# Optimization experiments

Hardware: AMD Instinct MI355X
Metric: run time of the kernel (lower is better)

Reference implementation:

```python
import jax, jax.numpy as jnp
import numpy as np

NU = 50000   # num user nodes
NI = 50000   # num item nodes
E = 1600000  # edges per relation
DIN = 256    # in_features
H = 8        # n_heads
F = 64       # out_features per head (hidden = H*F = 512)
NEG_SLOPE = 0.2


def setup_inputs() -> dict:
    key = jax.random.key(0)
    ks = jax.random.split(key, 14)
    wscale = 0.05
    return {
        "x_user": jax.random.normal(ks[0], (NU, DIN), jnp.float32),
        "x_item": jax.random.normal(ks[1], (NI, DIN), jnp.float32),
        "Wv": jax.random.normal(ks[2], (3, DIN, H * F), jnp.float32) * wscale,
        "bv": jax.random.normal(ks[3], (3, H * F), jnp.float32) * wscale,
        "Wq": jax.random.normal(ks[4], (3, H * F, H), jnp.float32) * wscale,
        "bq": jax.random.normal(ks[5], (3, H), jnp.float32) * wscale,
        "Wk": jax.random.normal(ks[6], (3, H * F, H), jnp.float32) * wscale,
        "bk": jax.random.normal(ks[7], (3, H), jnp.float32) * wscale,
        "src1": jax.random.randint(ks[8], (E,), 0, NU, jnp.int32),   # user -> item
        "dst1": jax.random.randint(ks[9], (E,), 0, NI, jnp.int32),
        "src2": jax.random.randint(ks[10], (E,), 0, NI, jnp.int32),  # item -> user
        "dst2": jax.random.randint(ks[11], (E,), 0, NU, jnp.int32),
        "src3": jax.random.randint(ks[12], (E,), 0, NU, jnp.int32),  # user -> user
        "dst3": jax.random.randint(ks[13], (E,), 0, NU, jnp.int32),
    }


def _gat_relation(x_src, x_dst, Wv, bv, Wq, bq, Wk, bk, src, dst, n_dst):
    # linear_v on src and dst node features: [N, H*F]
    h_src = x_src @ Wv + bv
    h_dst = x_dst @ Wv + bv
    q = h_dst @ Wq + bq  # [Nd, H] per-head query logit
    k = h_src @ Wk + bk  # [Ns, H] per-head key logit
    # fused_gsddmm: gather to edges, leaky_relu, segment softmax over dst
    e = jax.nn.leaky_relu(q[dst] + k[src], NEG_SLOPE)  # [E, H]
    m = jax.ops.segment_max(e, dst, num_segments=n_dst)  # [Nd, H]
    m = jnp.where(jnp.isfinite(m), m, jnp.zeros_like(m))
    ex = jnp.exp(e - m[dst])
    denom = jax.ops.segment_sum(ex, dst, num_segments=n_dst)  # [Nd, H]
    attn = ex / jnp.maximum(denom[dst], 1e-9)  # [E, H]
    # gspmm: attention-weighted scatter-sum of src features into dst
    hs = h_src.reshape(-1, H, F)  # [Ns, H, F]
    agg = jax.ops.segment_sum(attn[:, :, None] * hs[src], dst, num_segments=n_dst)  # [Nd, H, F]
    return agg.mean(axis=1)  # torch.mean(h, dim=1) -> [Nd, F]


def reference(x_user, x_item, Wv, bv, Wq, bq, Wk, bk, src1, dst1, src2, dst2, src3, dst3):
    # relation 0: user -> item
    out_item = _gat_relation(x_user, x_item, Wv[0], bv[0], Wq[0], bq[0], Wk[0], bk[0], src1, dst1, NI)
    # relations 1 (item -> user) and 2 (user -> user) both target user: mean over relations
    r1 = _gat_relation(x_item, x_user, Wv[1], bv[1], Wq[1], bq[1], Wk[1], bk[1], src2, dst2, NU)
    r2 = _gat_relation(x_user, x_user, Wv[2], bv[2], Wq[2], bq[2], Wk[2], bk[2], src3, dst3, NU)
    out_user = (r1 + r2) / 2.0
    return out_user, out_item
```

## Files before the change

### kernel.cpp

```cpp
#include <hip/hip_runtime.h>

typedef unsigned short u16;
typedef __attribute__((ext_vector_type(4))) float f32x4;
typedef __attribute__((ext_vector_type(8))) short s16x8;

#define NND 50000
#define EDG 1600000
#define NBK 391
#define TOTB (3 * NBK)
#define TS 4096
#define CAPB 5120

__device__ __forceinline__ u16 f2b(float f) {
  union { float f; unsigned u; } c; c.f = f;
  unsigned r = c.u + 0x7fff + ((c.u >> 16) & 1);
  return (u16)(r >> 16);
}

__device__ __forceinline__ void accum8(float* num, uint4 u, float4 w0, float4 w1) {
  num[0] += w0.x * __int_as_float((int)(u.x << 16));
  num[1] += w0.y * __int_as_float((int)(u.x & 0xFFFF0000u));
  num[2] += w0.z * __int_as_float((int)(u.y << 16));
  num[3] += w0.w * __int_as_float((int)(u.y & 0xFFFF0000u));
  num[4] += w1.x * __int_as_float((int)(u.z << 16));
  num[5] += w1.y * __int_as_float((int)(u.z & 0xFFFF0000u));
  num[6] += w1.z * __int_as_float((int)(u.w << 16));
  num[7] += w1.w * __int_as_float((int)(u.w & 0xFFFF0000u));
}

__global__ void k_prepw(const float* __restrict__ Wv, u16* __restrict__ Wt,
                        float* __restrict__ Wvt, int* __restrict__ bcur) {
  int tid = blockIdx.x * 256 + threadIdx.x;
  if (tid < 3 * 512 * 256) {
    int r = tid / (512 * 256); int rem = tid - r * 512 * 256;
    int n = rem >> 8; int kk = rem & 255;
    float v = Wv[((size_t)r * 256 + kk) * 512 + n];
    Wt[tid] = f2b(v);
    Wvt[tid] = v;
  }
  if (tid < TOTB) bcur[tid] = tid * CAPB;
}

__global__ void __launch_bounds__(256) k_fusew2(
    const float* __restrict__ Wvt, const float* __restrict__ bv,
    const float* __restrict__ Wq, const float* __restrict__ bq,
    const float* __restrict__ Wk, const float* __restrict__ bk,
    float* __restrict__ FW, float* __restrict__ FB) {
  __shared__ float red[256];
  int r = blockIdx.x >> 4, o = blockIdx.x & 15;
  int t = threadIdx.x;
  const float* wvt = Wvt + (size_t)r * 512 * 256;
  const float* wqk = (o < 8) ? (Wq + (size_t)r * 512 * 8 + o) : (Wk + (size_t)r * 512 * 8 + (o - 8));
  float acc = 0.f;
#pragma unroll 8
  for (int j = 0; j < 512; j++) acc += wvt[(size_t)j * 256 + t] * wqk[j * 8];
  FW[((size_t)r * 16 + o) * 256 + t] = acc;
  float pb = 0.f;
  for (int j = t; j < 512; j += 256) pb += bv[r * 512 + j] * wqk[j * 8];
  red[t] = pb;
  __syncthreads();
  for (int off = 128; off > 0; off >>= 1) {
    if (t < off) red[t] += red[t + off];
    __syncthreads();
  }
  if (t == 0) {
    float b = (o < 8) ? bq[r * 8 + o] : bk[r * 8 + (o - 8)];
    FB[r * 16 + o] = red[0] + b;
  }
}

__global__ void __launch_bounds__(256) kb_scatter(
    const int* __restrict__ s1, const int* __restrict__ d1,
    const int* __restrict__ s2, const int* __restrict__ d2,
    const int* __restrict__ s3, const int* __restrict__ d3,
    int* __restrict__ BCUR, unsigned* __restrict__ pairs) {
  __shared__ int h[NBK];
  __shared__ int bbase[NBK];
  int tid = threadIdx.x;
  int r = blockIdx.y;
  const int* dp = (r == 0) ? d1 : (r == 1) ? d2 : d3;
  const int* sp = (r == 0) ? s1 : (r == 1) ? s2 : s3;
  int e0 = blockIdx.x * TS;
  int n = EDG - e0; if (n > TS) n = TS;
  for (int b = tid; b < NBK; b += 256) h[b] = 0;
  __syncthreads();
  int eb[16]; unsigned ev[16];
#pragma unroll
  for (int k = 0; k < 16; k++) {
    int i = k * 256 + tid;
    if (i < n) {
      int d = dp[e0 + i], ss = sp[e0 + i];
      eb[k] = d >> 7;
      ev[k] = ((unsigned)(d & 127) << 16) | (unsigned)ss;
      atomicAdd(&h[eb[k]], 1);
    } else eb[k] = -1;
  }
  __syncthreads();
  for (int b = tid; b < NBK; b += 256) {
    int c = h[b];
    bbase[b] = c ? atomicAdd(&BCUR[r * NBK + b], c) : 0;
  }
  __syncthreads();
  for (int b = tid; b < NBK; b += 256) h[b] = 0;
  __syncthreads();
#pragma unroll
  for (int k = 0; k < 16; k++) {
    if (eb[k] >= 0) {
      int off = atomicAdd(&h[eb[k]], 1);
      int pos = bbase[eb[k]] + off;
      int limit = (r * NBK + eb[k] + 1) * CAPB;
      if (pos < limit) pairs[pos] = ev[k];
    }
  }
}

__global__ void __launch_bounds__(256) kb_build(
    const unsigned* __restrict__ pairs, const int* __restrict__ BCUR,
    int* __restrict__ rp, int* __restrict__ dgarr, u16* __restrict__ csrc) {
  __shared__ int cntl[128];
  __shared__ int sc[128];
  __shared__ int curl[128];
  int t = threadIdx.x;
  int r = blockIdx.y, bx = blockIdx.x;
  int bin = r * NBK + bx;
  int base = bin * CAPB;
  int cnt = BCUR[bin] - base; if (cnt > CAPB) cnt = CAPB;
  int node0 = bx << 7;
  int nloc = NND - node0; if (nloc > 128) nloc = 128;
  if (t < 128) cntl[t] = 0;
  __syncthreads();
  for (int i = t; i < cnt; i += 256)
    atomicAdd(&cntl[pairs[base + i] >> 16], 1);
  __syncthreads();
  if (t < 128) sc[t] = cntl[t];
  __syncthreads();
  for (int off = 1; off < 128; off <<= 1) {
    int v = 0;
    if (t < 128) { v = sc[t]; if (t >= off) v += sc[t - off]; }
    __syncthreads();
    if (t < 128) sc[t] = v;
    __syncthreads();
  }
  if (t < 128) {
    int excl = sc[t] - cntl[t];
    if (t < nloc) { rp[r * NND + node0 + t] = base + excl; dgarr[r * NND + node0 + t] = cntl[t]; }
    curl[t] = base + excl;
  }
  __syncthreads();
  for (int i = t; i < cnt; i += 256) {
    unsigned v = pairs[base + i];
    int p = atomicAdd(&curl[v >> 16], 1);
    csrc[p] = (u16)(v & 0xFFFFu);
  }
}

__global__ void __launch_bounds__(256) k_gemm(const float* __restrict__ A, const u16* __restrict__ Bt,
                                              const float* __restrict__ bias, u16* __restrict__ C, int M) {
  __shared__ u16 sA[128 * 72];
  __shared__ u16 sB[128 * 72];
  int tid = threadIdx.x;
  int lane = tid & 63, wid = tid >> 6;
  int wm = wid >> 1, wn = wid & 1;
  int l15 = lane & 15, l4 = lane >> 4;
  int m0 = blockIdx.x * 128, n0 = blockIdx.y * 128;
  f32x4 acc[4][4] = {};
  for (int ko = 0; ko < 256; ko += 64) {
#pragma unroll
    for (int p = 0; p < 4; p++) {
      int idx = p * 256 + tid;
      int row = idx >> 3, seg = idx & 7;
      int gm = m0 + row; if (gm >= M) gm = M - 1;
      float4 a0 = *(const float4*)(A + (size_t)gm * 256 + ko + seg * 8);
      float4 a1 = *(const float4*)(A + (size_t)gm * 256 + ko + seg * 8 + 4);
      s16x8 av;
      av[0] = (short)f2b(a0.x); av[1] = (short)f2b(a0.y);
      av[2] = (short)f2b(a0.z); av[3] = (short)f2b(a0.w);
      av[4] = (short)f2b(a1.x); av[5] = (short)f2b(a1.y);
      av[6] = (short)f2b(a1.z); av[7] = (short)f2b(a1.w);
      *(s16x8*)&sA[row * 72 + seg * 8] = av;
      *(s16x8*)&sB[row * 72 + seg * 8] = *(const s16x8*)(Bt + (n0 + row) * 256 + ko + seg * 8);
    }
    __syncthreads();
#pragma unroll
    for (int kk = 0; kk < 2; kk++) {
      s16x8 af[4], bf[4];
#pragma unroll
      for (int i = 0; i < 4; i++) af[i] = *(const s16x8*)&sA[(wm * 64 + i * 16 + l15) * 72 + kk * 32 + l4 * 8];
#pragma unroll
      for (int j = 0; j < 4; j++) bf[j] = *(const s16x8*)&sB[(wn * 64 + j * 16 + l15) * 72 + kk * 32 + l4 * 8];
#pragma unroll
      for (int i = 0; i < 4; i++)
#pragma unroll
        for (int j = 0; j < 4; j++)
          acc[i][j] = __builtin_amdgcn_mfma_f32_16x16x32_bf16(af[i], bf[j], acc[i][j], 0, 0, 0);
    }
    __syncthreads();
  }
#pragma unroll
  for (int j = 0; j < 4; j++) {
    int n = n0 + wn * 64 + j * 16 + l15;
    float bb = bias[n];
    int tpos = ((n & 63) << 3) + (n >> 6);
#pragma unroll
    for (int i = 0; i < 4; i++) {
      int mb = m0 + wm * 64 + i * 16 + l4 * 4;
#pragma unroll
      for (int r = 0; r < 4; r++) {
        int m = mb + r;
        if (m < M) C[(size_t)m * 512 + tpos] = f2b(acc[i][j][r] + bb);
      }
    }
  }
}

__global__ void __launch_bounds__(256) k_qk(
    const float* __restrict__ xu, const float* __restrict__ xi,
    const float* __restrict__ FW, const float* __restrict__ FB,
    float* __restrict__ K0, float* __restrict__ Q1, float* __restrict__ Q2,
    float* __restrict__ K2, float* __restrict__ Q0, float* __restrict__ K1) {
  int lane = threadIdx.x & 63, wid = threadIdx.x >> 6;
  if (blockIdx.x < 1024) {
    int stride = 1024 * 4;
    for (int row = blockIdx.x * 4 + wid; row < NND; row += stride) {
      float4 xv = *(const float4*)(xu + (size_t)row * 256 + lane * 4);
      {
        float p[16];
#pragma unroll
        for (int c = 0; c < 16; c++) {
          const float4 wv = *(const float4*)(FW + (size_t)(8 + c) * 256 + lane * 4);
          p[c] = xv.x * wv.x + xv.y * wv.y + xv.z * wv.z + xv.w * wv.w;
        }
#pragma unroll
        for (int off = 1; off < 64; off <<= 1)
#pragma unroll
          for (int c = 0; c < 16; c++) p[c] += __shfl_xor(p[c], off, 64);
        if (lane == 0) {
#pragma unroll
          for (int c = 0; c < 8; c++) K0[row * 8 + c] = p[c] + FB[8 + c];
#pragma unroll
          for (int c = 0; c < 8; c++) Q1[row * 8 + c] = p[8 + c] + FB[16 + c];
        }
      }
      {
        float p[16];
#pragma unroll
        for (int c = 0; c < 16; c++) {
          const float4 wv = *(const float4*)(FW + (size_t)(32 + c) * 256 + lane * 4);
          p[c] = xv.x * wv.x + xv.y * wv.y + xv.z * wv.z + xv.w * wv.w;
        }
#pragma unroll
        for (int off = 1; off < 64; off <<= 1)
#pragma unroll
          for (int c = 0; c < 16; c++) p[c] += __shfl_xor(p[c], off, 64);
        if (lane == 0) {
#pragma unroll
          for (int c = 0; c < 8; c++) Q2[row * 8 + c] = p[c] + FB[32 + c];
#pragma unroll
          for (int c = 0; c < 8; c++) K2[row * 8 + c] = p[8 + c] + FB[40 + c];
        }
      }
    }
  } else {
    int b = blockIdx.x - 1024;
    int stride = 512 * 4;
    for (int row = b * 4 + wid; row < NND; row += stride) {
      float4 xv = *(const float4*)(xi + (size_t)row * 256 + lane * 4);
      float p[16];
#pragma unroll
      for (int c = 0; c < 16; c++) {
        const float4 wv = *(const float4*)(FW + (size_t)((c < 8) ? c : (16 + c)) * 256 + lane * 4);
        p[c] = xv.x * wv.x + xv.y * wv.y + xv.z * wv.z + xv.w * wv.w;
      }
#pragma unroll
      for (int off = 1; off < 64; off <<= 1)
#pragma unroll
        for (int c = 0; c < 16; c++) p[c] += __shfl_xor(p[c], off, 64);
      if (lane == 0) {
#pragma unroll
        for (int c = 0; c < 8; c++) Q0[row * 8 + c] = p[c] + FB[c];
#pragma unroll
        for (int c = 0; c < 8; c++) K1[row * 8 + c] = p[8 + c] + FB[24 + c];
      }
    }
  }
}

__global__ void __launch_bounds__(256) k_edge(
    const int* __restrict__ rp, const int* __restrict__ dg, const u16* __restrict__ csrc,
    const float* __restrict__ q, const float* __restrict__ k,
    const u16* __restrict__ hs, float* __restrict__ out,
    float scale, int accum) {
  __shared__ float exw[4][64 * 8];
  __shared__ int sarr[4][64];
  __shared__ float sd[4][8];
  __shared__ float sacc[4][64];
  int lane = threadIdx.x & 63, w = threadIdx.x >> 6;
  int dst = blockIdx.x * 2 + (w >> 1);
  int half = w & 1;
  int beg = rp[dst];
  int deg = dg[dst];
  int hlen = (deg + 1) >> 1;
  int s0 = half ? hlen : 0;
  int s1 = half ? deg : hlen;
  float qv[8];
  {
    float4 q0 = *(const float4*)(q + dst * 8);
    float4 q1 = *(const float4*)(q + dst * 8 + 4);
    qv[0] = q0.x; qv[1] = q0.y; qv[2] = q0.z; qv[3] = q0.w;
    qv[4] = q1.x; qv[5] = q1.y; qv[6] = q1.z; qv[7] = q1.w;
  }
  float num[8] = {0, 0, 0, 0, 0, 0, 0, 0};
  float dsum[8] = {0, 0, 0, 0, 0, 0, 0, 0};
  for (int base = s0; base < s1; base += 64) {
    int i = base + lane;
    int nn = min(64, s1 - base);
    if (i < s1) {
      int s = (int)csrc[beg + i];
      sarr[w][lane] = s;
      float4 k0 = *(const float4*)(k + s * 8);
      float4 k1 = *(const float4*)(k + s * 8 + 4);
      float kv[8] = {k0.x, k0.y, k0.z, k0.w, k1.x, k1.y, k1.z, k1.w};
#pragma unroll
      for (int h = 0; h < 8; h++) {
        float e = qv[h] + kv[h];
        e = e > 0.f ? e : 0.2f * e;
        float wgt = exp2f(e * 1.44269504f);
        exw[w][lane * 8 + h] = wgt;
        dsum[h] += wgt;
      }
    }
    __asm__ __volatile__("s_waitcnt lgkmcnt(0)" ::: "memory");
    int j = 0;
    for (; j + 4 <= nn; j += 4) {
      int sa = sarr[w][j], sb = sarr[w][j + 1], sc = sarr[w][j + 2], sdn = sarr[w][j + 3];
      uint4 ua = *(const uint4*)(hs + (size_t)sa * 512 + lane * 8);
      uint4 ub = *(const uint4*)(hs + (size_t)sb * 512 + lane * 8);
      uint4 uc = *(const uint4*)(hs + (size_t)sc * 512 + lane * 8);
      uint4 ud = *(const uint4*)(hs + (size_t)sdn * 512 + lane * 8);
      float4 wa0 = *(const float4*)&exw[w][j * 8],       wa1 = *(const float4*)&exw[w][j * 8 + 4];
      float4 wb0 = *(const float4*)&exw[w][j * 8 + 8],   wb1 = *(const float4*)&exw[w][j * 8 + 12];
      float4 wc0 = *(const float4*)&exw[w][j * 8 + 16],  wc1 = *(const float4*)&exw[w][j * 8 + 20];
      float4 wd0 = *(const float4*)&exw[w][j * 8 + 24],  wd1 = *(const float4*)&exw[w][j * 8 + 28];
      accum8(num, ua, wa0, wa1);
      accum8(num, ub, wb0, wb1);
      accum8(num, uc, wc0, wc1);
      accum8(num, ud, wd0, wd1);
    }
    for (; j < nn; j++) {
      int s = sarr[w][j];
      uint4 u = *(const uint4*)(hs + (size_t)s * 512 + lane * 8);
      float4 e0 = *(const float4*)&exw[w][j * 8];
      float4 e1 = *(const float4*)&exw[w][j * 8 + 4];
      accum8(num, u, e0, e1);
    }
  }
#pragma unroll
  for (int off = 1; off < 64; off <<= 1)
#pragma unroll
    for (int h = 0; h < 8; h++) dsum[h] += __shfl_xor(dsum[h], off, 64);
  if (lane == 0) {
#pragma unroll
    for (int h = 0; h < 8; h++) sd[w][h] = dsum[h];
  }
  __syncthreads();
  float acc = 0.f;
#pragma unroll
  for (int h = 0; h < 8; h++) {
    float tot = sd[w][h] + sd[w ^ 1][h];
    float rden = tot > 0.f ? 1.f / tot : 0.f;
    acc += num[h] * rden;
  }
  acc *= scale;
  sacc[w][lane] = acc;
  __syncthreads();
  if (half == 0) {
    float tot = sacc[w][lane] + sacc[w + 1][lane];
    if (accum) out[dst * 64 + lane] += tot;
    else out[dst * 64 + lane] = tot;
  }
}

extern "C" void kernel_launch(void* const* d_in, const int* in_sizes, int n_in,
                              void* d_out, int out_size, void* d_ws, size_t ws_size,
                              hipStream_t stream) {
  const float* xu = (const float*)d_in[0];
  const float* xi = (const float*)d_in[1];
  const float* Wv = (const float*)d_in[2];
  const float* bv = (const float*)d_in[3];
  const float* Wq = (const float*)d_in[4];
  const float* bq = (const float*)d_in[5];
  const float* Wk = (const float*)d_in[6];
  const float* bk = (const float*)d_in[7];
  const int* src1 = (const int*)d_in[8];
  const int* dst1 = (const int*)d_in[9];
  const int* src2 = (const int*)d_in[10];
  const int* dst2 = (const int*)d_in[11];
  const int* src3 = (const int*)d_in[12];
  const int* dst3 = (const int*)d_in[13];
  float* out_user = (float*)d_out;
  float* out_item = out_user + (size_t)NND * 64;

  char* w = (char*)d_ws;
  auto alloc = [&](size_t sz) -> char* {
    char* p = w; w += (sz + 255) & ~(size_t)255; return p;
  };
  u16* H     = (u16*)alloc((size_t)NND * 512 * 2);
  u16* WT    = (u16*)alloc((size_t)3 * 512 * 256 * 2);
  float* WVT = (float*)alloc((size_t)3 * 512 * 256 * 4);
  float* FW  = (float*)alloc((size_t)3 * 16 * 256 * 4);
  float* FB  = (float*)alloc((size_t)3 * 16 * 4);
  float* Q0 = (float*)alloc((size_t)NND * 8 * 4);
  float* K0 = (float*)alloc((size_t)NND * 8 * 4);
  float* Q1 = (float*)alloc((size_t)NND * 8 * 4);
  float* K1 = (float*)alloc((size_t)NND * 8 * 4);
  float* Q2 = (float*)alloc((size_t)NND * 8 * 4);
  float* K2 = (float*)alloc((size_t)NND * 8 * 4);
  int* ROWPTR = (int*)alloc((size_t)3 * NND * 4);
  int* DEG    = (int*)alloc((size_t)3 * NND * 4);
  int* BCUR   = (int*)alloc(TOTB * 4);
  u16* CSRC   = (u16*)alloc((size_t)TOTB * CAPB * 2);
  unsigned* PAIRS = (unsigned*)H;
  (void)ws_size; (void)n_in; (void)in_sizes; (void)out_size;

  k_prepw<<<(3 * 512 * 256 + 255) / 256, 256, 0, stream>>>(Wv, WT, WVT, BCUR);

  kb_scatter<<<dim3((EDG + TS - 1) / TS, 3), 256, 0, stream>>>(src1, dst1, src2, dst2, src3, dst3, BCUR, PAIRS);
  kb_build<<<dim3(NBK, 3), 256, 0, stream>>>(PAIRS, BCUR, ROWPTR, DEG, CSRC);

  k_fusew2<<<48, 256, 0, stream>>>(WVT, bv, Wq, bq, Wk, bk, FW, FB);
  k_qk<<<1536, 256, 0, stream>>>(xu, xi, FW, FB, K0, Q1, Q2, K2, Q0, K1);

  dim3 gg((NND + 127) / 128, 4);
  k_gemm<<<gg, 256, 0, stream>>>(xu, WT,                 bv,        H, NND);
  k_edge<<<NND / 2, 256, 0, stream>>>(ROWPTR,           DEG,           CSRC, Q0, K0, H, out_item, 0.125f,  0);
  k_gemm<<<gg, 256, 0, stream>>>(xi, WT + 512 * 256,     bv + 512,  H, NND);
  k_edge<<<NND / 2, 256, 0, stream>>>(ROWPTR + NND,     DEG + NND,     CSRC, Q1, K1, H, out_user, 0.0625f, 0);
  k_gemm<<<gg, 256, 0, stream>>>(xu, WT + 2 * 512 * 256, bv + 1024, H, NND);
  k_edge<<<NND / 2, 256, 0, stream>>>(ROWPTR + 2 * NND, DEG + 2 * NND, CSRC, Q2, K2, H, out_user, 0.0625f, 1);
}
```

Before: 1.209 ms.

## Co-schedule next relation's GEMM with current edge aggregation via double-buffered H

Adds a second bf16 projection buffer so the GEMM for relation r+1 can run in the same launch as the edge aggregation for relation r, with a block-index split that dispatches each block to either the GEMM body or the edge body. The first GEMM is likewise merged with the Q/K projection kernel. The aim is to overlap the compute-bound MFMA GEMM with the memory-bound gather, and to cut launch count and tail idle time. In exchange it uses more workspace, shares LDS through a union, and falls back to the old sequence when the workspace is too small.

```diff
diff --git a/kernel.cpp b/kernel.cpp
--- a/kernel.cpp
+++ b/kernel.cpp
@@ -10,6 +10,9 @@
 #define TOTB (3 * NBK)
 #define TS 4096
 #define CAPB 5120
+#define GEMMB (NBK * 4)
+#define QKB 1536
+#define EDGEB (NND / 2)
 
 __device__ __forceinline__ u16 f2b(float f) {
   union { float f; unsigned u; } c; c.f = f;
@@ -26,6 +29,237 @@
   num[5] += w1.y * __int_as_float((int)(u.z & 0xFFFF0000u));
   num[6] += w1.z * __int_as_float((int)(u.w << 16));
   num[7] += w1.w * __int_as_float((int)(u.w & 0xFFFF0000u));
+}
+
+struct EdgeSmem {
+  float exw[4][512];
+  int sarr[4][64];
+  float sd[4][8];
+  float sacc[4][64];
+};
+struct GemmSmem {
+  u16 sA[128 * 72];
+  u16 sB[128 * 72];
+};
+union Smem { EdgeSmem e; GemmSmem g; };
+
+__device__ void gemm_body(GemmSmem& sm, const float* __restrict__ A, const u16* __restrict__ Bt,
+                          const float* __restrict__ bias, u16* __restrict__ C, int bx) {
+  int tid = threadIdx.x;
+  int lane = tid & 63, wid = tid >> 6;
+  int wm = wid >> 1, wn = wid & 1;
+  int l15 = lane & 15, l4 = lane >> 4;
+  int m0 = (bx >> 2) * 128, n0 = (bx & 3) * 128;
+  f32x4 acc[4][4] = {};
+  for (int ko = 0; ko < 256; ko += 64) {
+#pragma unroll
+    for (int p = 0; p < 4; p++) {
+      int idx = p * 256 + tid;
+      int row = idx >> 3, seg = idx & 7;
+      int gm = m0 + row; if (gm >= NND) gm = NND - 1;
+      float4 a0 = *(const float4*)(A + (size_t)gm * 256 + ko + seg * 8);
+      float4 a1 = *(const float4*)(A + (size_t)gm * 256 + ko + seg * 8 + 4);
+      s16x8 av;
+      av[0] = (short)f2b(a0.x); av[1] = (short)f2b(a0.y);
+      av[2] = (short)f2b(a0.z); av[3] = (short)f2b(a0.w);
+      av[4] = (short)f2b(a1.x); av[5] = (short)f2b(a1.y);
+      av[6] = (short)f2b(a1.z); av[7] = (short)f2b(a1.w);
+      *(s16x8*)&sm.sA[row * 72 + seg * 8] = av;
+      *(s16x8*)&sm.sB[row * 72 + seg * 8] = *(const s16x8*)(Bt + (size_t)(n0 + row) * 256 + ko + seg * 8);
+    }
+    __syncthreads();
+#pragma unroll
+    for (int kk = 0; kk < 2; kk++) {
+      s16x8 af[4], bf[4];
+#pragma unroll
+      for (int i = 0; i < 4; i++) af[i] = *(const s16x8*)&sm.sA[(wm * 64 + i * 16 + l15) * 72 + kk * 32 + l4 * 8];
+#pragma unroll
+      for (int j = 0; j < 4; j++) bf[j] = *(const s16x8*)&sm.sB[(wn * 64 + j * 16 + l15) * 72 + kk * 32 + l4 * 8];
+#pragma unroll
+      for (int i = 0; i < 4; i++)
+#pragma unroll
+        for (int j = 0; j < 4; j++)
+          acc[i][j] = __builtin_amdgcn_mfma_f32_16x16x32_bf16(af[i], bf[j], acc[i][j], 0, 0, 0);
+    }
+    __syncthreads();
+  }
+#pragma unroll
+  for (int j = 0; j < 4; j++) {
+    int n = n0 + wn * 64 + j * 16 + l15;
+    float bb = bias[n];
+    int tpos = ((n & 63) << 3) + (n >> 6);
+#pragma unroll
+    for (int i = 0; i < 4; i++) {
+      int mb = m0 + wm * 64 + i * 16 + l4 * 4;
+#pragma unroll
+      for (int r = 0; r < 4; r++) {
+        int m = mb + r;
+        if (m < NND) C[(size_t)m * 512 + tpos] = f2b(acc[i][j][r] + bb);
+      }
+    }
+  }
+}
+
+__device__ void edge_body(EdgeSmem& sm, int bx,
+                          const int* __restrict__ rp, const int* __restrict__ dg,
+                          const u16* __restrict__ csrc, const float* __restrict__ q,
+                          const float* __restrict__ k, const u16* __restrict__ hs,
+                          float* __restrict__ out, float scale, int accum) {
+  int lane = threadIdx.x & 63, w = threadIdx.x >> 6;
+  int dst = bx * 2 + (w >> 1);
+  int half = w & 1;
+  int beg = rp[dst];
+  int deg = dg[dst];
+  int hlen = (deg + 1) >> 1;
+  int s0 = half ? hlen : 0;
+  int s1 = half ? deg : hlen;
+  float qv[8];
+  {
+    float4 q0 = *(const float4*)(q + dst * 8);
+    float4 q1 = *(const float4*)(q + dst * 8 + 4);
+    qv[0] = q0.x; qv[1] = q0.y; qv[2] = q0.z; qv[3] = q0.w;
+    qv[4] = q1.x; qv[5] = q1.y; qv[6] = q1.z; qv[7] = q1.w;
+  }
+  float num[8] = {0, 0, 0, 0, 0, 0, 0, 0};
+  float dsum[8] = {0, 0, 0, 0, 0, 0, 0, 0};
+  for (int base = s0; base < s1; base += 64) {
+    int i = base + lane;
+    int nn = min(64, s1 - base);
+    if (i < s1) {
+      int s = (int)csrc[beg + i];
+      sm.sarr[w][lane] = s;
+      float4 k0 = *(const float4*)(k + s * 8);
+      float4 k1 = *(const float4*)(k + s * 8 + 4);
+      float kv[8] = {k0.x, k0.y, k0.z, k0.w, k1.x, k1.y, k1.z, k1.w};
+#pragma unroll
+      for (int h = 0; h < 8; h++) {
+        float e = qv[h] + kv[h];
+        e = e > 0.f ? e : 0.2f * e;
+        float wgt = exp2f(e * 1.44269504f);
+        sm.exw[w][lane * 8 + h] = wgt;
+        dsum[h] += wgt;
+      }
+    }
+    __asm__ __volatile__("s_waitcnt lgkmcnt(0)" ::: "memory");
+    int j = 0;
+    for (; j + 4 <= nn; j += 4) {
+      int sa = sm.sarr[w][j], sb = sm.sarr[w][j + 1], sc = sm.sarr[w][j + 2], sdn = sm.sarr[w][j + 3];
+      uint4 ua = *(const uint4*)(hs + (size_t)sa * 512 + lane * 8);
+      uint4 ub = *(const uint4*)(hs + (size_t)sb * 512 + lane * 8);
+      uint4 uc = *(const uint4*)(hs + (size_t)sc * 512 + lane * 8);
+      uint4 ud = *(const uint4*)(hs + (size_t)sdn * 512 + lane * 8);
+      float4 wa0 = *(const float4*)&sm.exw[w][j * 8],       wa1 = *(const float4*)&sm.exw[w][j * 8 + 4];
+      float4 wb0 = *(const float4*)&sm.exw[w][j * 8 + 8],   wb1 = *(const float4*)&sm.exw[w][j * 8 + 12];
+      float4 wc0 = *(const float4*)&sm.exw[w][j * 8 + 16],  wc1 = *(const float4*)&sm.exw[w][j * 8 + 20];
+      float4 wd0 = *(const float4*)&sm.exw[w][j * 8 + 24],  wd1 = *(const float4*)&sm.exw[w][j * 8 + 28];
+      accum8(num, ua, wa0, wa1);
+      accum8(num, ub, wb0, wb1);
+      accum8(num, uc, wc0, wc1);
+      accum8(num, ud, wd0, wd1);
+    }
+    for (; j < nn; j++) {
+      int s = sm.sarr[w][j];
+      uint4 u = *(const uint4*)(hs + (size_t)s * 512 + lane * 8);
+      float4 e0 = *(const float4*)&sm.exw[w][j * 8];
+      float4 e1 = *(const float4*)&sm.exw[w][j * 8 + 4];
+      accum8(num, u, e0, e1);
+    }
+  }
+#pragma unroll
+  for (int off = 1; off < 64; off <<= 1)
+#pragma unroll
+    for (int h = 0; h < 8; h++) dsum[h] += __shfl_xor(dsum[h], off, 64);
+  if (lane == 0) {
+#pragma unroll
+    for (int h = 0; h < 8; h++) sm.sd[w][h] = dsum[h];
+  }
+  __syncthreads();
+  float acc = 0.f;
+#pragma unroll
+  for (int h = 0; h < 8; h++) {
+    float tot = sm.sd[w][h] + sm.sd[w ^ 1][h];
+    float rden = tot > 0.f ? 1.f / tot : 0.f;
+    acc += num[h] * rden;
+  }
+  acc *= scale;
+  sm.sacc[w][lane] = acc;
+  __syncthreads();
+  if (half == 0) {
+    float tot = sm.sacc[w][lane] + sm.sacc[w + 1][lane];
+    if (accum) out[dst * 64 + lane] += tot;
+    else out[dst * 64 + lane] = tot;
+  }
+}
+
+__device__ void qk_body(int qb, const float* __restrict__ xu, const float* __restrict__ xi,
+                        const float* __restrict__ FW, const float* __restrict__ FB,
+                        float* __restrict__ K0, float* __restrict__ Q1, float* __restrict__ Q2,
+                        float* __restrict__ K2, float* __restrict__ Q0, float* __restrict__ K1) {
+  int lane = threadIdx.x & 63, wid = threadIdx.x >> 6;
+  if (qb < 1024) {
+    int stride = 1024 * 4;
+    for (int row = qb * 4 + wid; row < NND; row += stride) {
+      float4 xv = *(const float4*)(xu + (size_t)row * 256 + lane * 4);
+      {
+        float p[16];
+#pragma unroll
+        for (int c = 0; c < 16; c++) {
+          const float4 wv = *(const float4*)(FW + (size_t)(8 + c) * 256 + lane * 4);
+          p[c] = xv.x * wv.x + xv.y * wv.y + xv.z * wv.z + xv.w * wv.w;
+        }
+#pragma unroll
+        for (int off = 1; off < 64; off <<= 1)
+#pragma unroll
+          for (int c = 0; c < 16; c++) p[c] += __shfl_xor(p[c], off, 64);
+        if (lane == 0) {
+#pragma unroll
+          for (int c = 0; c < 8; c++) K0[row * 8 + c] = p[c] + FB[8 + c];
+#pragma unroll
+          for (int c = 0; c < 8; c++) Q1[row * 8 + c] = p[8 + c] + FB[16 + c];
+        }
+      }
+      {
+        float p[16];
+#pragma unroll
+        for (int c = 0; c < 16; c++) {
+          const float4 wv = *(const float4*)(FW + (size_t)(32 + c) * 256 + lane * 4);
+          p[c] = xv.x * wv.x + xv.y * wv.y + xv.z * wv.z + xv.w * wv.w;
+        }
+#pragma unroll
+        for (int off = 1; off < 64; off <<= 1)
+#pragma unroll
+          for (int c = 0; c < 16; c++) p[c] += __shfl_xor(p[c], off, 64);
+        if (lane == 0) {
+#pragma unroll
+          for (int c = 0; c < 8; c++) Q2[row * 8 + c] = p[c] + FB[32 + c];
+#pragma unroll
+          for (int c = 0; c < 8; c++) K2[row * 8 + c] = p[8 + c] + FB[40 + c];
+        }
+      }
+    }
+  } else {
+    int b = qb - 1024;
+    int stride = 512 * 4;
+    for (int row = b * 4 + wid; row < NND; row += stride) {
+      float4 xv = *(const float4*)(xi + (size_t)row * 256 + lane * 4);
+      float p[16];
+#pragma unroll
+      for (int c = 0; c < 16; c++) {
+        const float4 wv = *(const float4*)(FW + (size_t)((c < 8) ? c : (16 + c)) * 256 + lane * 4);
+        p[c] = xv.x * wv.x + xv.y * wv.y + xv.z * wv.z + xv.w * wv.w;
+      }
+#pragma unroll
+      for (int off = 1; off < 64; off <<= 1)
+#pragma unroll
+        for (int c = 0; c < 16; c++) p[c] += __shfl_xor(p[c], off, 64);
+      if (lane == 0) {
+#pragma unroll
+        for (int c = 0; c < 8; c++) Q0[row * 8 + c] = p[c] + FB[c];
+#pragma unroll
+        for (int c = 0; c < 8; c++) K1[row * 8 + c] = p[8 + c] + FB[24 + c];
+      }
+    }
+  }
 }
 
 __global__ void k_prepw(const float* __restrict__ Wv, u16* __restrict__ Wt,
@@ -155,62 +389,9 @@
 }
 
 __global__ void __launch_bounds__(256) k_gemm(const float* __restrict__ A, const u16* __restrict__ Bt,
-                                              const float* __restrict__ bias, u16* __restrict__ C, int M) {
-  __shared__ u16 sA[128 * 72];
-  __shared__ u16 sB[128 * 72];
-  int tid = threadIdx.x;
-  int lane = tid & 63, wid = tid >> 6;
-  int wm = wid >> 1, wn = wid & 1;
-  int l15 = lane & 15, l4 = lane >> 4;
-  int m0 = blockIdx.x * 128, n0 = blockIdx.y * 128;
-  f32x4 acc[4][4] = {};
-  for (int ko = 0; ko < 256; ko += 64) {
-#pragma unroll
-    for (int p = 0; p < 4; p++) {
-      int idx = p * 256 + tid;
-      int row = idx >> 3, seg = idx & 7;
-      int gm = m0 + row; if (gm >= M) gm = M - 1;
-      float4 a0 = *(const float4*)(A + (size_t)gm * 256 + ko + seg * 8);
-      float4 a1 = *(const float4*)(A + (size_t)gm * 256 + ko + seg * 8 + 4);
-      s16x8 av;
-      av[0] = (short)f2b(a0.x); av[1] = (short)f2b(a0.y);
-      av[2] = (short)f2b(a0.z); av[3] = (short)f2b(a0.w);
-      av[4] = (short)f2b(a1.x); av[5] = (short)f2b(a1.y);
-      av[6] = (short)f2b(a1.z); av[7] = (short)f2b(a1.w);
-      *(s16x8*)&sA[row * 72 + seg * 8] = av;
-      *(s16x8*)&sB[row * 72 + seg * 8] = *(const s16x8*)(Bt + (n0 + row) * 256 + ko + seg * 8);
-    }
-    __syncthreads();
-#pragma unroll
-    for (int kk = 0; kk < 2; kk++) {
-      s16x8 af[4], bf[4];
-#pragma unroll
-      for (int i = 0; i < 4; i++) af[i] = *(const s16x8*)&sA[(wm * 64 + i * 16 + l15) * 72 + kk * 32 + l4 * 8];
-#pragma unroll
-      for (int j = 0; j < 4; j++) bf[j] = *(const s16x8*)&sB[(wn * 64 + j * 16 + l15) * 72 + kk * 32 + l4 * 8];
-#pragma unroll
-      for (int i = 0; i < 4; i++)
-#pragma unroll
-        for (int j = 0; j < 4; j++)
-          acc[i][j] = __builtin_amdgcn_mfma_f32_16x16x32_bf16(af[i], bf[j], acc[i][j], 0, 0, 0);
-    }
-    __syncthreads();
-  }
-#pragma unroll
-  for (int j = 0; j < 4; j++) {
-    int n = n0 + wn * 64 + j * 16 + l15;
-    float bb = bias[n];
-    int tpos = ((n & 63) << 3) + (n >> 6);
-#pragma unroll
-    for (int i = 0; i < 4; i++) {
-      int mb = m0 + wm * 64 + i * 16 + l4 * 4;
-#pragma unroll
-      for (int r = 0; r < 4; r++) {
-        int m = mb + r;
-        if (m < M) C[(size_t)m * 512 + tpos] = f2b(acc[i][j][r] + bb);
-      }
-    }
-  }
+                                              const float* __restrict__ bias, u16* __restrict__ C) {
+  __shared__ GemmSmem sm;
+  gemm_body(sm, A, Bt, bias, C, blockIdx.x);
 }
 
 __global__ void __launch_bounds__(256) k_qk(
@@ -218,166 +399,38 @@
     const float* __restrict__ FW, const float* __restrict__ FB,
     float* __restrict__ K0, float* __restrict__ Q1, float* __restrict__ Q2,
     float* __restrict__ K2, float* __restrict__ Q0, float* __restrict__ K1) {
-  int lane = threadIdx.x & 63, wid = threadIdx.x >> 6;
-  if (blockIdx.x < 1024) {
-    int stride = 1024 * 4;
-    for (int row = blockIdx.x * 4 + wid; row < NND; row += stride) {
-      float4 xv = *(const float4*)(xu + (size_t)row * 256 + lane * 4);
-      {
-        float p[16];
-#pragma unroll
-        for (int c = 0; c < 16; c++) {
-          const float4 wv = *(const float4*)(FW + (size_t)(8 + c) * 256 + lane * 4);
-          p[c] = xv.x * wv.x + xv.y * wv.y + xv.z * wv.z + xv.w * wv.w;
-        }
-#pragma unroll
-        for (int off = 1; off < 64; off <<= 1)
-#pragma unroll
-          for (int c = 0; c < 16; c++) p[c] += __shfl_xor(p[c], off, 64);
-        if (lane == 0) {
-#pragma unroll
-          for (int c = 0; c < 8; c++) K0[row * 8 + c] = p[c] + FB[8 + c];
-#pragma unroll
-          for (int c = 0; c < 8; c++) Q1[row * 8 + c] = p[8 + c] + FB[16 + c];
-        }
-      }
-      {
-        float p[16];
-#pragma unroll
-        for (int c = 0; c < 16; c++) {
-          const float4 wv = *(const float4*)(FW + (size_t)(32 + c) * 256 + lane * 4);
-          p[c] = xv.x * wv.x + xv.y * wv.y + xv.z * wv.z + xv.w * wv.w;
-        }
-#pragma unroll
-        for (int off = 1; off < 64; off <<= 1)
-#pragma unroll
-          for (int c = 0; c < 16; c++) p[c] += __shfl_xor(p[c], off, 64);
-        if (lane == 0) {
-#pragma unroll
-          for (int c = 0; c < 8; c++) Q2[row * 8 + c] = p[c] + FB[32 + c];
-#pragma unroll
-          for (int c = 0; c < 8; c++) K2[row * 8 + c] = p[8 + c] + FB[40 + c];
-        }
-      }
-    }
-  } else {
-    int b = blockIdx.x - 1024;
-    int stride = 512 * 4;
-    for (int row = b * 4 + wid; row < NND; row += stride) {
-      float4 xv = *(const float4*)(xi + (size_t)row * 256 + lane * 4);
-      float p[16];
-#pragma unroll
-      for (int c = 0; c < 16; c++) {
-        const float4 wv = *(const float4*)(FW + (size_t)((c < 8) ? c : (16 + c)) * 256 + lane * 4);
-        p[c] = xv.x * wv.x + xv.y * wv.y + xv.z * wv.z + xv.w * wv.w;
-      }
-#pragma unroll
-      for (int off = 1; off < 64; off <<= 1)
-#pragma unroll
-        for (int c = 0; c < 16; c++) p[c] += __shfl_xor(p[c], off, 64);
-      if (lane == 0) {
-#pragma unroll
-        for (int c = 0; c < 8; c++) Q0[row * 8 + c] = p[c] + FB[c];
-#pragma unroll
-        for (int c = 0; c < 8; c++) K1[row * 8 + c] = p[8 + c] + FB[24 + c];
-      }
-    }
-  }
+  qk_body(blockIdx.x, xu, xi, FW, FB, K0, Q1, Q2, K2, Q0, K1);
 }
 
 __global__ void __launch_bounds__(256) k_edge(
     const int* __restrict__ rp, const int* __restrict__ dg, const u16* __restrict__ csrc,
     const float* __restrict__ q, const float* __restrict__ k,
-    const u16* __restrict__ hs, float* __restrict__ out,
-    float scale, int accum) {
-  __shared__ float exw[4][64 * 8];
-  __shared__ int sarr[4][64];
-  __shared__ float sd[4][8];
-  __shared__ float sacc[4][64];
-  int lane = threadIdx.x & 63, w = threadIdx.x >> 6;
-  int dst = blockIdx.x * 2 + (w >> 1);
-  int half = w & 1;
-  int beg = rp[dst];
-  int deg = dg[dst];
-  int hlen = (deg + 1) >> 1;
-  int s0 = half ? hlen : 0;
-  int s1 = half ? deg : hlen;
-  float qv[8];
-  {
-    float4 q0 = *(const float4*)(q + dst * 8);
-    float4 q1 = *(const float4*)(q + dst * 8 + 4);
-    qv[0] = q0.x; qv[1] = q0.y; qv[2] = q0.z; qv[3] = q0.w;
-    qv[4] = q1.x; qv[5] = q1.y; qv[6] = q1.z; qv[7] = q1.w;
-  }
-  float num[8] = {0, 0, 0, 0, 0, 0, 0, 0};
-  float dsum[8] = {0, 0, 0, 0, 0, 0, 0, 0};
-  for (int base = s0; base < s1; base += 64) {
-    int i = base + lane;
-    int nn = min(64, s1 - base);
-    if (i < s1) {
-      int s = (int)csrc[beg + i];
-      sarr[w][lane] = s;
-      float4 k0 = *(const float4*)(k + s * 8);
-      float4 k1 = *(const float4*)(k + s * 8 + 4);
-      float kv[8] = {k0.x, k0.y, k0.z, k0.w, k1.x, k1.y, k1.z, k1.w};
-#pragma unroll
-      for (int h = 0; h < 8; h++) {
-        float e = qv[h] + kv[h];
-        e = e > 0.f ? e : 0.2f * e;
-        float wgt = exp2f(e * 1.44269504f);
-        exw[w][lane * 8 + h] = wgt;
-        dsum[h] += wgt;
-      }
-    }
-    __asm__ __volatile__("s_waitcnt lgkmcnt(0)" ::: "memory");
-    int j = 0;
-    for (; j + 4 <= nn; j += 4) {
-      int sa = sarr[w][j], sb = sarr[w][j + 1], sc = sarr[w][j + 2], sdn = sarr[w][j + 3];
-      uint4 ua = *(const uint4*)(hs + (size_t)sa * 512 + lane * 8);
-      uint4 ub = *(const uint4*)(hs + (size_t)sb * 512 + lane * 8);
-      uint4 uc = *(const uint4*)(hs + (size_t)sc * 512 + lane * 8);
-      uint4 ud = *(const uint4*)(hs + (size_t)sdn * 512 + lane * 8);
-      float4 wa0 = *(const float4*)&exw[w][j * 8],       wa1 = *(const float4*)&exw[w][j * 8 + 4];
-      float4 wb0 = *(const float4*)&exw[w][j * 8 + 8],   wb1 = *(const float4*)&exw[w][j * 8 + 12];
-      float4 wc0 = *(const float4*)&exw[w][j * 8 + 16],  wc1 = *(const float4*)&exw[w][j * 8 + 20];
-      float4 wd0 = *(const float4*)&exw[w][j * 8 + 24],  wd1 = *(const float4*)&exw[w][j * 8 + 28];
-      accum8(num, ua, wa0, wa1);
-      accum8(num, ub, wb0, wb1);
-      accum8(num, uc, wc0, wc1);
-      accum8(num, ud, wd0, wd1);
-    }
-    for (; j < nn; j++) {
-      int s = sarr[w][j];
-      uint4 u = *(const uint4*)(hs + (size_t)s * 512 + lane * 8);
-      float4 e0 = *(const float4*)&exw[w][j * 8];
-      float4 e1 = *(const float4*)&exw[w][j * 8 + 4];
-      accum8(num, u, e0, e1);
-    }
-  }
-#pragma unroll
-  for (int off = 1; off < 64; off <<= 1)
-#pragma unroll
-    for (int h = 0; h < 8; h++) dsum[h] += __shfl_xor(dsum[h], off, 64);
-  if (lane == 0) {
-#pragma unroll
-    for (int h = 0; h < 8; h++) sd[w][h] = dsum[h];
-  }
-  __syncthreads();
-  float acc = 0.f;
-#pragma unroll
-  for (int h = 0; h < 8; h++) {
-    float tot = sd[w][h] + sd[w ^ 1][h];
-    float rden = tot > 0.f ? 1.f / tot : 0.f;
-    acc += num[h] * rden;
-  }
-  acc *= scale;
-  sacc[w][lane] = acc;
-  __syncthreads();
-  if (half == 0) {
-    float tot = sacc[w][lane] + sacc[w + 1][lane];
-    if (accum) out[dst * 64 + lane] += tot;
-    else out[dst * 64 + lane] = tot;
-  }
+    const u16* __restrict__ hs, float* __restrict__ out, float scale, int accum) {
+  __shared__ EdgeSmem sm;
+  edge_body(sm, blockIdx.x, rp, dg, csrc, q, k, hs, out, scale, accum);
+}
+
+__global__ void __launch_bounds__(256) k_gemm_qk(
+    const float* __restrict__ A, const u16* __restrict__ Bt, const float* __restrict__ bias,
+    u16* __restrict__ C,
+    const float* __restrict__ xu, const float* __restrict__ xi,
+    const float* __restrict__ FW, const float* __restrict__ FB,
+    float* __restrict__ K0, float* __restrict__ Q1, float* __restrict__ Q2,
+    float* __restrict__ K2, float* __restrict__ Q0, float* __restrict__ K1) {
+  __shared__ Smem sm;
+  if ((int)blockIdx.x < GEMMB) gemm_body(sm.g, A, Bt, bias, C, blockIdx.x);
+  else qk_body(blockIdx.x - GEMMB, xu, xi, FW, FB, K0, Q1, Q2, K2, Q0, K1);
+}
+
+__global__ void __launch_bounds__(256) k_edge_gemm(
+    const int* __restrict__ rp, const int* __restrict__ dg, const u16* __restrict__ csrc,
+    const float* __restrict__ q, const float* __restrict__ k,
+    const u16* __restrict__ hread, float* __restrict__ out, float scale, int accum,
+    const float* __restrict__ A, const u16* __restrict__ Bt, const float* __restrict__ bias,
+    u16* __restrict__ hwrite) {
+  __shared__ Smem sm;
+  if ((int)blockIdx.x < GEMMB) gemm_body(sm.g, A, Bt, bias, hwrite, blockIdx.x);
+  else edge_body(sm.e, blockIdx.x - GEMMB, rp, dg, csrc, q, k, hread, out, scale, accum);
 }
 
 extern "C" void kernel_launch(void* const* d_in, const int* in_sizes, int n_in,
@@ -404,7 +457,7 @@
   auto alloc = [&](size_t sz) -> char* {
     char* p = w; w += (sz + 255) & ~(size_t)255; return p;
   };
-  u16* H     = (u16*)alloc((size_t)NND * 512 * 2);
+  u16* H0    = (u16*)alloc((size_t)NND * 512 * 2);
   u16* WT    = (u16*)alloc((size_t)3 * 512 * 256 * 2);
   float* WVT = (float*)alloc((size_t)3 * 512 * 256 * 4);
   float* FW  = (float*)alloc((size_t)3 * 16 * 256 * 4);
@@ -419,22 +472,32 @@
   int* DEG    = (int*)alloc((size_t)3 * NND * 4);
   int* BCUR   = (int*)alloc(TOTB * 4);
   u16* CSRC   = (u16*)alloc((size_t)TOTB * CAPB * 2);
-  unsigned* PAIRS = (unsigned*)H;
-  (void)ws_size; (void)n_in; (void)in_sizes; (void)out_size;
+  u16* H1     = (u16*)alloc((size_t)NND * 512 * 2);
+  size_t used_dual = (size_t)(w - (char*)d_ws);
+  int dual = (ws_size == 0) || (ws_size >= used_dual);
+  unsigned* PAIRS = (unsigned*)H0;
+  (void)n_in; (void)in_sizes; (void)out_size;
 
   k_prepw<<<(3 * 512 * 256 + 255) / 256, 256, 0, stream>>>(Wv, WT, WVT, BCUR);
-
   kb_scatter<<<dim3((EDG + TS - 1) / TS, 3), 256, 0, stream>>>(src1, dst1, src2, dst2, src3, dst3, BCUR, PAIRS);
   kb_build<<<dim3(NBK, 3), 256, 0, stream>>>(PAIRS, BCUR, ROWPTR, DEG, CSRC);
-
   k_fusew2<<<48, 256, 0, stream>>>(WVT, bv, Wq, bq, Wk, bk, FW, FB);
-  k_qk<<<1536, 256, 0, stream>>>(xu, xi, FW, FB, K0, Q1, Q2, K2, Q0, K1);
-
-  dim3 gg((NND + 127) / 128, 4);
-  k_gemm<<<gg, 256, 0, stream>>>(xu, WT,                 bv,        H, NND);
-  k_edge<<<NND / 2, 256, 0, stream>>>(ROWPTR,           DEG,           CSRC, Q0, K0, H, out_item, 0.125f,  0);
-  k_gemm<<<gg, 256, 0, stream>>>(xi, WT + 512 * 256,     bv + 512,  H, NND);
-  k_edge<<<NND / 2, 256, 0, stream>>>(ROWPTR + NND,     DEG + NND,     CSRC, Q1, K1, H, out_user, 0.0625f, 0);
-  k_gemm<<<gg, 256, 0, stream>>>(xu, WT + 2 * 512 * 256, bv + 1024, H, NND);
-  k_edge<<<NND / 2, 256, 0, stream>>>(ROWPTR + 2 * NND, DEG + 2 * NND, CSRC, Q2, K2, H, out_user, 0.0625f, 1);
-}
+
+  if (dual) {
+    k_gemm_qk<<<GEMMB + QKB, 256, 0, stream>>>(xu, WT, bv, H0,
+                                               xu, xi, FW, FB, K0, Q1, Q2, K2, Q0, K1);
+    k_edge_gemm<<<GEMMB + EDGEB, 256, 0, stream>>>(ROWPTR, DEG, CSRC, Q0, K0, H0, out_item, 0.125f, 0,
+                                                   xi, WT + 512 * 256, bv + 512, H1);
+    k_edge_gemm<<<GEMMB + EDGEB, 256, 0, stream>>>(ROWPTR + NND, DEG + NND, CSRC, Q1, K1, H1, out_user, 0.0625f, 0,
+                                                   xu, WT + 2 * 512 * 256, bv + 1024, H0);
+    k_edge<<<EDGEB, 256, 0, stream>>>(ROWPTR + 2 * NND, DEG + 2 * NND, CSRC, Q2, K2, H0, out_user, 0.0625f, 1);
+  } else {
+    k_qk<<<GEMMB ? 1536 : 1536, 256, 0, stream>>>(xu, xi, FW, FB, K0, Q1, Q2, K2, Q0, K1);
+    k_gemm<<<GEMMB, 256, 0, stream>>>(xu, WT, bv, H0);
+    k_edge<<<EDGEB, 256, 0, stream>>>(ROWPTR, DEG, CSRC, Q0, K0, H0, out_item, 0.125f, 0);
+    k_gemm<<<GEMMB, 256, 0, stream>>>(xi, WT + 512 * 256, bv + 512, H0);
+    k_edge<<<EDGEB, 256, 0, stream>>>(ROWPTR + NND, DEG + NND, CSRC, Q1, K1, H0, out_user, 0.0625f, 0);
+    k_gemm<<<GEMMB, 256, 0, stream>>>(xu, WT + 2 * 512 * 256, bv + 1024, H0);
+    k_edge<<<EDGEB, 256, 0, stream>>>(ROWPTR + 2 * NND, DEG + 2 * NND, CSRC, Q2, K2, H0, out_user, 0.0625f, 1);
+  }
+}
```

After: 2.167 ms. 1.79x slower.

## Stage full A row-tile in LDS once and loop over all N tiles

Applied to the files above, without the earlier changes.

The GEMM now loads and converts a 128x256 fp32 A tile to bf16 in shared memory once per block, then iterates over the four 128-column output tiles inside the block. This removes the fourfold re-reading and re-conversion of A across the former N-dimension grid. In exchange the grid shrinks to 391 blocks and shared memory use per block grows substantially, which lowers occupancy and parallelism.

```diff
diff --git a/kernel.cpp b/kernel.cpp
--- a/kernel.cpp
+++ b/kernel.cpp
@@ -10,6 +10,7 @@
 #define TOTB (3 * NBK)
 #define TS 4096
 #define CAPB 5120
+#define SAST 264
 
 __device__ __forceinline__ u16 f2b(float f) {
   union { float f; unsigned u; } c; c.f = f;
@@ -155,59 +156,68 @@
 }
 
 __global__ void __launch_bounds__(256) k_gemm(const float* __restrict__ A, const u16* __restrict__ Bt,
-                                              const float* __restrict__ bias, u16* __restrict__ C, int M) {
-  __shared__ u16 sA[128 * 72];
+                                              const float* __restrict__ bias, u16* __restrict__ C) {
+  __shared__ u16 sA[128 * SAST];
   __shared__ u16 sB[128 * 72];
   int tid = threadIdx.x;
   int lane = tid & 63, wid = tid >> 6;
   int wm = wid >> 1, wn = wid & 1;
   int l15 = lane & 15, l4 = lane >> 4;
-  int m0 = blockIdx.x * 128, n0 = blockIdx.y * 128;
-  f32x4 acc[4][4] = {};
-  for (int ko = 0; ko < 256; ko += 64) {
-#pragma unroll
-    for (int p = 0; p < 4; p++) {
-      int idx = p * 256 + tid;
-      int row = idx >> 3, seg = idx & 7;
-      int gm = m0 + row; if (gm >= M) gm = M - 1;
-      float4 a0 = *(const float4*)(A + (size_t)gm * 256 + ko + seg * 8);
-      float4 a1 = *(const float4*)(A + (size_t)gm * 256 + ko + seg * 8 + 4);
-      s16x8 av;
-      av[0] = (short)f2b(a0.x); av[1] = (short)f2b(a0.y);
-      av[2] = (short)f2b(a0.z); av[3] = (short)f2b(a0.w);
-      av[4] = (short)f2b(a1.x); av[5] = (short)f2b(a1.y);
-      av[6] = (short)f2b(a1.z); av[7] = (short)f2b(a1.w);
-      *(s16x8*)&sA[row * 72 + seg * 8] = av;
-      *(s16x8*)&sB[row * 72 + seg * 8] = *(const s16x8*)(Bt + (n0 + row) * 256 + ko + seg * 8);
-    }
-    __syncthreads();
-#pragma unroll
-    for (int kk = 0; kk < 2; kk++) {
-      s16x8 af[4], bf[4];
-#pragma unroll
-      for (int i = 0; i < 4; i++) af[i] = *(const s16x8*)&sA[(wm * 64 + i * 16 + l15) * 72 + kk * 32 + l4 * 8];
-#pragma unroll
-      for (int j = 0; j < 4; j++) bf[j] = *(const s16x8*)&sB[(wn * 64 + j * 16 + l15) * 72 + kk * 32 + l4 * 8];
-#pragma unroll
-      for (int i = 0; i < 4; i++)
-#pragma unroll
-        for (int j = 0; j < 4; j++)
-          acc[i][j] = __builtin_amdgcn_mfma_f32_16x16x32_bf16(af[i], bf[j], acc[i][j], 0, 0, 0);
-    }
-    __syncthreads();
-  }
-#pragma unroll
-  for (int j = 0; j < 4; j++) {
-    int n = n0 + wn * 64 + j * 16 + l15;
-    float bb = bias[n];
-    int tpos = ((n & 63) << 3) + (n >> 6);
-#pragma unroll
-    for (int i = 0; i < 4; i++) {
-      int mb = m0 + wm * 64 + i * 16 + l4 * 4;
-#pragma unroll
-      for (int r = 0; r < 4; r++) {
-        int m = mb + r;
-        if (m < M) C[(size_t)m * 512 + tpos] = f2b(acc[i][j][r] + bb);
+  int m0 = blockIdx.x * 128;
+#pragma unroll
+  for (int p = 0; p < 16; p++) {
+    int idx = p * 256 + tid;
+    int row = idx >> 5, seg = idx & 31;
+    int gm = m0 + row; if (gm >= NND) gm = NND - 1;
+    float4 a0 = *(const float4*)(A + (size_t)gm * 256 + seg * 8);
+    float4 a1 = *(const float4*)(A + (size_t)gm * 256 + seg * 8 + 4);
+    s16x8 av;
+    av[0] = (short)f2b(a0.x); av[1] = (short)f2b(a0.y);
+    av[2] = (short)f2b(a0.z); av[3] = (short)f2b(a0.w);
+    av[4] = (short)f2b(a1.x); av[5] = (short)f2b(a1.y);
+    av[6] = (short)f2b(a1.z); av[7] = (short)f2b(a1.w);
+    *(s16x8*)&sA[row * SAST + seg * 8] = av;
+  }
+  __syncthreads();
+  for (int nt = 0; nt < 4; nt++) {
+    int n0 = nt * 128;
+    f32x4 acc[4][4] = {};
+    for (int ko = 0; ko < 256; ko += 64) {
+#pragma unroll
+      for (int p = 0; p < 4; p++) {
+        int idx = p * 256 + tid;
+        int row = idx >> 3, seg = idx & 7;
+        *(s16x8*)&sB[row * 72 + seg * 8] = *(const s16x8*)(Bt + (size_t)(n0 + row) * 256 + ko + seg * 8);
+      }
+      __syncthreads();
+#pragma unroll
+      for (int kk = 0; kk < 2; kk++) {
+        s16x8 af[4], bf[4];
+#pragma unroll
+        for (int i = 0; i < 4; i++) af[i] = *(const s16x8*)&sA[(wm * 64 + i * 16 + l15) * SAST + ko + kk * 32 + l4 * 8];
+#pragma unroll
+        for (int j = 0; j < 4; j++) bf[j] = *(const s16x8*)&sB[(wn * 64 + j * 16 + l15) * 72 + kk * 32 + l4 * 8];
+#pragma unroll
+        for (int i = 0; i < 4; i++)
+#pragma unroll
+          for (int j = 0; j < 4; j++)
+            acc[i][j] = __builtin_amdgcn_mfma_f32_16x16x32_bf16(af[i], bf[j], acc[i][j], 0, 0, 0);
+      }
+      __syncthreads();
+    }
+#pragma unroll
+    for (int j = 0; j < 4; j++) {
+      int n = n0 + wn * 64 + j * 16 + l15;
+      float bb = bias[n];
+      int tpos = ((n & 63) << 3) + (n >> 6);
+#pragma unroll
+      for (int i = 0; i < 4; i++) {
+        int mb = m0 + wm * 64 + i * 16 + l4 * 4;
+#pragma unroll
+        for (int r = 0; r < 4; r++) {
+          int m = mb + r;
+          if (m < NND) C[(size_t)m * 512 + tpos] = f2b(acc[i][j][r] + bb);
+        }
       }
     }
   }
@@ -430,11 +440,10 @@
   k_fusew2<<<48, 256, 0, stream>>>(WVT, bv, Wq, bq, Wk, bk, FW, FB);
   k_qk<<<1536, 256, 0, stream>>>(xu, xi, FW, FB, K0, Q1, Q2, K2, Q0, K1);
 
-  dim3 gg((NND + 127) / 128, 4);
-  k_gemm<<<gg, 256, 0, stream>>>(xu, WT,                 bv,        H, NND);
-  k_edge<<<NND / 2, 256, 0, stream>>>(ROWPTR,           DEG,           CSRC, Q0, K0, H, out_item, 0.125f,  0);
-  k_gemm<<<gg, 256, 0, stream>>>(xi, WT + 512 * 256,     bv + 512,  H, NND);
-  k_edge<<<NND / 2, 256, 0, stream>>>(ROWPTR + NND,     DEG + NND,     CSRC, Q1, K1, H, out_user, 0.0625f, 0);
-  k_gemm<<<gg, 256, 0, stream>>>(xu, WT + 2 * 512 * 256, bv + 1024, H, NND);
+  k_gemm<<<NBK, 256, 0, stream>>>(xu, WT, bv, H);
+  k_edge<<<NND / 2, 256, 0, stream>>>(ROWPTR, DEG, CSRC, Q0, K0, H, out_item, 0.125f, 0);
+  k_gemm<<<NBK, 256, 0, stream>>>(xi, WT + 512 * 256, bv + 512, H);
+  k_edge<<<NND / 2, 256, 0, stream>>>(ROWPTR + NND, DEG + NND, CSRC, Q1, K1, H, out_user, 0.0625f, 0);
+  k_gemm<<<NBK, 256, 0, stream>>>(xu, WT + 2 * 512 * 256, bv + 1024, H);
   k_edge<<<NND / 2, 256, 0, stream>>>(ROWPTR + 2 * NND, DEG + 2 * NND, CSRC, Q2, K2, H, out_user, 0.0625f, 1);
 }
```

New measurement: 1.255 ms. 3.8% more time.
